# Kernel tuning notes

Measured on AMD Instinct MI355X. Metric: run time of the kernel, lower is better.

Reference implementation:

```python
import jax, jax.numpy as jnp
import numpy as np

B, L, D, U = 4, 1024, 64, 32

def setup_inputs() -> dict:
    key = jax.random.key(0)
    ks = jax.random.split(key, 6)
    inputs = jax.random.normal(ks[0], (B, L, D), dtype=jnp.float32)
    Wt = jax.random.normal(ks[1], (D, U), dtype=jnp.float32) * 0.1
    Wx = jax.random.normal(ks[2], (D, U), dtype=jnp.float32) * 0.1
    Wa = jax.random.normal(ks[3], (U, 1), dtype=jnp.float32) * 0.1
    bh = jax.random.normal(ks[4], (U,), dtype=jnp.float32) * 0.1
    ba = jax.random.normal(ks[5], (1,), dtype=jnp.float32) * 0.1
    return {"inputs": inputs, "Wt": Wt, "Wx": Wx, "Wa": Wa,
            "bh": bh, "ba": ba, "attention_width": 0}

def reference(inputs, Wt, Wx, Wa, bh, ba, attention_width):
    # Additive (Bahdanau) self-attention emission.
    q = inputs @ Wt                              # (B, L, U)
    k = inputs @ Wx                              # (B, L, U)
    # broadcast add -> (B, L, L, U), the dominant intermediate
    h = jnp.tanh(q[:, :, None, :] + k[:, None, :, :] + bh)
    e = jnp.squeeze(h @ Wa, axis=-1) + ba        # (B, L, L); ba broadcasts
    # NOTE: attention_width mask is dead code in the original forward -> ignored.
    # manual max-subtracted softmax with +1e-8 denominator (as in source)
    m = jnp.max(e, axis=-1, keepdims=True)
    ex = jnp.exp(e - m)
    a = ex / (jnp.sum(ex, axis=-1, keepdims=True) + 1e-8)
    v = jnp.einsum('bij,bjd->bid', a, inputs)    # (B, L, D)
    return v
```

## Files before the change

kernel.cpp:

```cpp
#include <hip/hip_runtime.h>

#define BB 4
#define LL 1024
#define DD 64
#define UU 32
#define NW 4
#define NT 256
#define JH 512
#define NTILE 8

__global__ __launch_bounds__(256) void precompute_kernel(
    const float* __restrict__ inp, const float* __restrict__ Wx,
    float* __restrict__ Ekt)
{
    __shared__ float s_in[8][DD];
    __shared__ float s_wx[DD][UU];
    __shared__ float s_ek[8][36];
    int t = threadIdx.x;
    int row0 = blockIdx.x * 8;
    if (t < 128)
        ((float4*)s_in)[t] = ((const float4*)(inp + (size_t)row0 * DD))[t];
#pragma unroll
    for (int p = 0; p < 2; ++p)
        ((float4*)s_wx)[p * 256 + t] = ((const float4*)Wx)[p * 256 + t];
    __syncthreads();
    int r = t >> 5;
    int u = t & 31;
    float k = 0.f;
#pragma unroll
    for (int d = 0; d < DD; ++d)
        k = fmaf(s_in[r][d], s_wx[d][u], k);
    s_ek[r][u] = __expf(2.f * k);
    __syncthreads();
    if (t < 64) {
        int u4 = t >> 3, r2 = t & 7;
        float4 v = *(const float4*)(&s_ek[r2][u4 * 4]);
        size_t gr = row0 + r2;
        size_t bb_ = gr >> 10, l = gr & 1023;
        ((float4*)Ekt)[(bb_ * 8 + u4) * LL + l] = v;
    }
}

__global__ __launch_bounds__(NT) void attn_partial_kernel(
    const float* __restrict__ Ekt, const float* __restrict__ inp,
    const float* __restrict__ Wt, const float* __restrict__ Wa,
    const float* __restrict__ bh,
    float* __restrict__ po, float* __restrict__ pm, float* __restrict__ ps)
{
    __shared__ union {
        struct { float wt[DD][UU]; float in[NW][DD]; } pre;
        float a[NW][JH];
    } sh;
    __shared__ float  s_eq[NW][UU];
    __shared__ float4 s_v[NW][NW][16];

    int t    = threadIdx.x;
    int w    = t >> 6;
    int lane = t & 63;
    int bid  = blockIdx.x;
    int q    = bid >> 1;
    int h    = bid & 1;
    int b    = q >> 8;
    int i0   = (q & 255) * NW;
    int j0   = h * JH;

    if (t < 64)
        ((float4*)sh.pre.in)[t] =
            ((const float4*)(inp + (size_t)(b * LL + i0) * DD))[t];
    ((float4*)sh.pre.wt)[t]       = ((const float4*)Wt)[t];
    ((float4*)sh.pre.wt)[t + 256] = ((const float4*)Wt)[t + 256];
    __syncthreads();
    if (t < NW * UU) {
        int r = t >> 5, u = t & 31;
        float qq = 0.f;
#pragma unroll
        for (int d = 0; d < DD; ++d)
            qq = fmaf(sh.pre.in[r][d], sh.pre.wt[d][u], qq);
        s_eq[r][u] = __expf(2.f * (qq + bh[u]));
    }
    __syncthreads();

    float eqv = s_eq[w][lane & 31];
    float sq[UU];
#pragma unroll
    for (int u = 0; u < UU; ++u)
        sq[u] = __uint_as_float(
            __builtin_amdgcn_readlane(__float_as_uint(eqv), u));

    const float4* ektb = (const float4*)Ekt + (size_t)b * 8 * LL;
    float rmax = -3.4e38f;
#pragma unroll 2
    for (int tile = 0; tile < NTILE; ++tile) {
        int jj = j0 + tile * 64 + lane;
        float4 ek[8];
#pragma unroll
        for (int u4 = 0; u4 < 8; ++u4) ek[u4] = ektb[u4 * LL + jj];
        float acc = 0.f;
#pragma unroll
        for (int u4 = 0; u4 < 8; ++u4) {
            float4 wav = *(const float4*)(Wa + u4 * 4);
            float p  = fmaf(sq[u4 * 4 + 0], ek[u4].x, 1.f);
            float qq = fmaf(sq[u4 * 4 + 1], ek[u4].y, 1.f);
            float r  = fmaf(sq[u4 * 4 + 2], ek[u4].z, 1.f);
            float s  = fmaf(sq[u4 * 4 + 3], ek[u4].w, 1.f);
            float n01 = fmaf(wav.x, qq, wav.y * p);
            float n23 = fmaf(wav.z, s, wav.w * r);
            float pq = p * qq, rs = r * s;
            float num = fmaf(n01, rs, n23 * pq);
            acc = fmaf(num, __builtin_amdgcn_rcpf(pq * rs), acc);
        }
        float e = -2.f * acc;
        rmax = fmaxf(rmax, e);
        sh.a[w][tile * 64 + lane] = e;
    }

#pragma unroll
    for (int m2 = 32; m2 >= 1; m2 >>= 1)
        rmax = fmaxf(rmax, __shfl_xor(rmax, m2, 64));
    float sum = 0.f;
#pragma unroll
    for (int tile = 0; tile < NTILE; ++tile) {
        float e  = sh.a[w][tile * 64 + lane];
        float ex = __expf(e - rmax);
        sum += ex;
        sh.a[w][tile * 64 + lane] = ex;
    }
#pragma unroll
    for (int m2 = 32; m2 >= 1; m2 >>= 1)
        sum += __shfl_xor(sum, m2, 64);
    if (lane == 0) {
        pm[bid * NW + w] = rmax;
        ps[bid * NW + w] = sum;
    }
    __syncthreads();

    int dq = t & 15;
    int g  = t >> 4;
    const float4* inp4 = (const float4*)(inp + (size_t)b * LL * DD);
    float4 v[NW];
#pragma unroll
    for (int i = 0; i < NW; ++i) v[i] = (float4){0.f, 0.f, 0.f, 0.f};

#pragma unroll 4
    for (int jj = 0; jj < JH / 16; ++jj) {
        int jl = jj * 16 + g;
        float4 x  = inp4[(size_t)(j0 + jl) * 16 + dq];
        float a0 = sh.a[0][jl], a1 = sh.a[1][jl];
        float a2 = sh.a[2][jl], a3 = sh.a[3][jl];
        v[0].x = fmaf(a0, x.x, v[0].x); v[0].y = fmaf(a0, x.y, v[0].y);
        v[0].z = fmaf(a0, x.z, v[0].z); v[0].w = fmaf(a0, x.w, v[0].w);
        v[1].x = fmaf(a1, x.x, v[1].x); v[1].y = fmaf(a1, x.y, v[1].y);
        v[1].z = fmaf(a1, x.z, v[1].z); v[1].w = fmaf(a1, x.w, v[1].w);
        v[2].x = fmaf(a2, x.x, v[2].x); v[2].y = fmaf(a2, x.y, v[2].y);
        v[2].z = fmaf(a2, x.z, v[2].z); v[2].w = fmaf(a2, x.w, v[2].w);
        v[3].x = fmaf(a3, x.x, v[3].x); v[3].y = fmaf(a3, x.y, v[3].y);
        v[3].z = fmaf(a3, x.z, v[3].z); v[3].w = fmaf(a3, x.w, v[3].w);
    }

#pragma unroll
    for (int i = 0; i < NW; ++i) {
        v[i].x += __shfl_xor(v[i].x, 16, 64); v[i].y += __shfl_xor(v[i].y, 16, 64);
        v[i].z += __shfl_xor(v[i].z, 16, 64); v[i].w += __shfl_xor(v[i].w, 16, 64);
        v[i].x += __shfl_xor(v[i].x, 32, 64); v[i].y += __shfl_xor(v[i].y, 32, 64);
        v[i].z += __shfl_xor(v[i].z, 32, 64); v[i].w += __shfl_xor(v[i].w, 32, 64);
    }
    if (lane < 16) {
#pragma unroll
        for (int i = 0; i < NW; ++i) s_v[w][i][dq] = v[i];
    }
    __syncthreads();

    int i = t >> 6;
    int d = t & 63;
    const float* svf = (const float*)s_v;
    float r = 0.f;
#pragma unroll
    for (int w2 = 0; w2 < NW; ++w2) r += svf[w2 * (NW * 64) + i * 64 + d];
    po[(size_t)bid * (NW * DD) + i * DD + d] = r;
}

__global__ __launch_bounds__(256) void combine_kernel(
    const float* __restrict__ po, const float* __restrict__ pm,
    const float* __restrict__ ps, float* __restrict__ out)
{
    int gid = blockIdx.x * 256 + threadIdx.x;
    int d   = gid & 63;
    int row = gid >> 6;
    int q   = row >> 2;
    int i   = row & 3;
    int b0  = q * 2, b1 = q * 2 + 1;
    float m0 = pm[b0 * NW + i], m1 = pm[b1 * NW + i];
    float s0 = ps[b0 * NW + i], s1 = ps[b1 * NW + i];
    float m  = fmaxf(m0, m1);
    float w0 = __expf(m0 - m), w1 = __expf(m1 - m);
    float s  = fmaf(s0, w0, s1 * w1) + 1e-8f;
    float o0 = po[(size_t)b0 * (NW * DD) + i * DD + d];
    float o1 = po[(size_t)b1 * (NW * DD) + i * DD + d];
    out[(size_t)row * DD + d] = fmaf(o0, w0, o1 * w1) * __builtin_amdgcn_rcpf(s);
}

extern "C" void kernel_launch(void* const* d_in, const int* in_sizes, int n_in,
                              void* d_out, int out_size, void* d_ws, size_t ws_size,
                              hipStream_t stream) {
    const float* inp = (const float*)d_in[0];
    const float* Wt  = (const float*)d_in[1];
    const float* Wx  = (const float*)d_in[2];
    const float* Wa  = (const float*)d_in[3];
    const float* bh  = (const float*)d_in[4];
    float* out = (float*)d_out;

    float* Ekt = (float*)d_ws;
    float* po  = Ekt + (size_t)BB * LL * UU;
    float* pm  = po + (size_t)2048 * NW * DD;
    float* ps  = pm + (size_t)2048 * NW;

    precompute_kernel<<<BB * LL / 8, 256, 0, stream>>>(inp, Wx, Ekt);
    attn_partial_kernel<<<2 * BB * LL / NW, NT, 0, stream>>>(
        Ekt, inp, Wt, Wa, bh, po, pm, ps);
    combine_kernel<<<BB * LL * DD / 256, 256, 0, stream>>>(po, pm, ps, out);
}
```

Measured before the change: 99.71 us.

## Store key exponentials row-major and keep softmax energies in registers

Changes the precomputed exp(2k) buffer from a transposed float4 layout to a plain row-major (row, unit) layout, so the precompute kernel writes directly without shared-memory staging. In the attention kernel, energies are kept in a register array for the max/exp/sum passes instead of being written to and re-read from shared memory. The normalized weights are then stored transposed as [j][row], so the value-accumulation loop fetches one float4 instead of four scalars. Each lane now reads a contiguous 128-byte row, which changes global load coalescing across lanes and adds register pressure.

```diff
diff --git a/kernel.cpp b/kernel.cpp
--- a/kernel.cpp
+++ b/kernel.cpp
@@ -11,11 +11,10 @@
 
 __global__ __launch_bounds__(256) void precompute_kernel(
     const float* __restrict__ inp, const float* __restrict__ Wx,
-    float* __restrict__ Ekt)
+    float* __restrict__ Ek)
 {
     __shared__ float s_in[8][DD];
     __shared__ float s_wx[DD][UU];
-    __shared__ float s_ek[8][36];
     int t = threadIdx.x;
     int row0 = blockIdx.x * 8;
     if (t < 128)
@@ -30,27 +29,21 @@
 #pragma unroll
     for (int d = 0; d < DD; ++d)
         k = fmaf(s_in[r][d], s_wx[d][u], k);
-    s_ek[r][u] = __expf(2.f * k);
-    __syncthreads();
-    if (t < 64) {
-        int u4 = t >> 3, r2 = t & 7;
-        float4 v = *(const float4*)(&s_ek[r2][u4 * 4]);
-        size_t gr = row0 + r2;
-        size_t bb_ = gr >> 10, l = gr & 1023;
-        ((float4*)Ekt)[(bb_ * 8 + u4) * LL + l] = v;
-    }
-}
+    Ek[(size_t)(row0 + r) * UU + u] = __expf(2.f * k);
+}
+
+union ShMem {
+    struct { float wt[DD][UU]; float in[NW][DD]; } pre;
+    float at[JH][NW];
+};
 
 __global__ __launch_bounds__(NT) void attn_partial_kernel(
-    const float* __restrict__ Ekt, const float* __restrict__ inp,
+    const float* __restrict__ Ek, const float* __restrict__ inp,
     const float* __restrict__ Wt, const float* __restrict__ Wa,
     const float* __restrict__ bh,
     float* __restrict__ po, float* __restrict__ pm, float* __restrict__ ps)
 {
-    __shared__ union {
-        struct { float wt[DD][UU]; float in[NW][DD]; } pre;
-        float a[NW][JH];
-    } sh;
+    __shared__ ShMem sh;
     __shared__ float  s_eq[NW][UU];
     __shared__ float4 s_v[NW][NW][16];
 
@@ -87,14 +80,15 @@
         sq[u] = __uint_as_float(
             __builtin_amdgcn_readlane(__float_as_uint(eqv), u));
 
-    const float4* ektb = (const float4*)Ekt + (size_t)b * 8 * LL;
-    float rmax = -3.4e38f;
+    const float* ekb = Ek + ((size_t)(b * LL) + j0) * UU;
+    float e[NTILE];
 #pragma unroll 2
     for (int tile = 0; tile < NTILE; ++tile) {
-        int jj = j0 + tile * 64 + lane;
+        const float4* ekp =
+            (const float4*)(ekb + (size_t)(tile * 64 + lane) * UU);
         float4 ek[8];
 #pragma unroll
-        for (int u4 = 0; u4 < 8; ++u4) ek[u4] = ektb[u4 * LL + jj];
+        for (int u4 = 0; u4 < 8; ++u4) ek[u4] = ekp[u4];
         float acc = 0.f;
 #pragma unroll
         for (int u4 = 0; u4 < 8; ++u4) {
@@ -109,21 +103,20 @@
             float num = fmaf(n01, rs, n23 * pq);
             acc = fmaf(num, __builtin_amdgcn_rcpf(pq * rs), acc);
         }
-        float e = -2.f * acc;
-        rmax = fmaxf(rmax, e);
-        sh.a[w][tile * 64 + lane] = e;
-    }
-
+        e[tile] = -2.f * acc;
+    }
+
+    float rmax = e[0];
+#pragma unroll
+    for (int tile = 1; tile < NTILE; ++tile) rmax = fmaxf(rmax, e[tile]);
 #pragma unroll
     for (int m2 = 32; m2 >= 1; m2 >>= 1)
         rmax = fmaxf(rmax, __shfl_xor(rmax, m2, 64));
     float sum = 0.f;
 #pragma unroll
     for (int tile = 0; tile < NTILE; ++tile) {
-        float e  = sh.a[w][tile * 64 + lane];
-        float ex = __expf(e - rmax);
-        sum += ex;
-        sh.a[w][tile * 64 + lane] = ex;
+        e[tile] = __expf(e[tile] - rmax);
+        sum += e[tile];
     }
 #pragma unroll
     for (int m2 = 32; m2 >= 1; m2 >>= 1)
@@ -132,6 +125,10 @@
         pm[bid * NW + w] = rmax;
         ps[bid * NW + w] = sum;
     }
+
+#pragma unroll
+    for (int tile = 0; tile < NTILE; ++tile)
+        sh.at[tile * 64 + lane][w] = e[tile];
     __syncthreads();
 
     int dq = t & 15;
@@ -144,17 +141,16 @@
 #pragma unroll 4
     for (int jj = 0; jj < JH / 16; ++jj) {
         int jl = jj * 16 + g;
-        float4 x  = inp4[(size_t)(j0 + jl) * 16 + dq];
-        float a0 = sh.a[0][jl], a1 = sh.a[1][jl];
-        float a2 = sh.a[2][jl], a3 = sh.a[3][jl];
-        v[0].x = fmaf(a0, x.x, v[0].x); v[0].y = fmaf(a0, x.y, v[0].y);
-        v[0].z = fmaf(a0, x.z, v[0].z); v[0].w = fmaf(a0, x.w, v[0].w);
-        v[1].x = fmaf(a1, x.x, v[1].x); v[1].y = fmaf(a1, x.y, v[1].y);
-        v[1].z = fmaf(a1, x.z, v[1].z); v[1].w = fmaf(a1, x.w, v[1].w);
-        v[2].x = fmaf(a2, x.x, v[2].x); v[2].y = fmaf(a2, x.y, v[2].y);
-        v[2].z = fmaf(a2, x.z, v[2].z); v[2].w = fmaf(a2, x.w, v[2].w);
-        v[3].x = fmaf(a3, x.x, v[3].x); v[3].y = fmaf(a3, x.y, v[3].y);
-        v[3].z = fmaf(a3, x.z, v[3].z); v[3].w = fmaf(a3, x.w, v[3].w);
+        float4 x = inp4[(size_t)(j0 + jl) * 16 + dq];
+        float4 a = *(const float4*)(&sh.at[jl][0]);
+        v[0].x = fmaf(a.x, x.x, v[0].x); v[0].y = fmaf(a.x, x.y, v[0].y);
+        v[0].z = fmaf(a.x, x.z, v[0].z); v[0].w = fmaf(a.x, x.w, v[0].w);
+        v[1].x = fmaf(a.y, x.x, v[1].x); v[1].y = fmaf(a.y, x.y, v[1].y);
+        v[1].z = fmaf(a.y, x.z, v[1].z); v[1].w = fmaf(a.y, x.w, v[1].w);
+        v[2].x = fmaf(a.z, x.x, v[2].x); v[2].y = fmaf(a.z, x.y, v[2].y);
+        v[2].z = fmaf(a.z, x.z, v[2].z); v[2].w = fmaf(a.z, x.w, v[2].w);
+        v[3].x = fmaf(a.w, x.x, v[3].x); v[3].y = fmaf(a.w, x.y, v[3].y);
+        v[3].z = fmaf(a.w, x.z, v[3].z); v[3].w = fmaf(a.w, x.w, v[3].w);
     }
 
 #pragma unroll
@@ -209,13 +205,13 @@
     const float* bh  = (const float*)d_in[4];
     float* out = (float*)d_out;
 
-    float* Ekt = (float*)d_ws;
-    float* po  = Ekt + (size_t)BB * LL * UU;
+    float* Ek  = (float*)d_ws;
+    float* po  = Ek + (size_t)BB * LL * UU;
     float* pm  = po + (size_t)2048 * NW * DD;
     float* ps  = pm + (size_t)2048 * NW;
 
-    precompute_kernel<<<BB * LL / 8, 256, 0, stream>>>(inp, Wx, Ekt);
+    precompute_kernel<<<BB * LL / 8, 256, 0, stream>>>(inp, Wx, Ek);
     attn_partial_kernel<<<2 * BB * LL / NW, NT, 0, stream>>>(
-        Ekt, inp, Wt, Wa, bh, po, pm, ps);
+        Ek, inp, Wt, Wa, bh, po, pm, ps);
     combine_kernel<<<BB * LL * DD / 256, 256, 0, stream>>>(po, pm, ps, out);
 }
```

Result: slower. 139.5 us (+39.9%).
